# Optimization experiments

Measured on AMD Instinct MI355X. Metric: run time of the kernel, lower is better.

The kernel has to match this reference:

```python
import jax, jax.numpy as jnp
import numpy as np

DAYS = 10
EPS = 1e-5


def _ln(x, g, b, axis):
    # LayerNorm over a single axis with affine params of shape (x.shape[axis],)
    m = x.mean(axis=axis, keepdims=True)
    v = ((x - m) ** 2).mean(axis=axis, keepdims=True)
    xn = (x - m) * jax.lax.rsqrt(v + EPS)
    shp = [1] * x.ndim
    shp[axis] = x.shape[axis]
    return xn * g.reshape(shp) + b.reshape(shp)


def setup_inputs() -> dict:
    B, T, C = 8192, 30, 64
    H = 30  # lstm hidden
    P = C * (C - 1) // 2  # 2016 pairwise channels
    CH1 = 2 * P + 5 * C + 7 * C  # 4800
    ks = jax.random.split(jax.random.key(0), 16)
    s = 0.05
    x = jax.random.uniform(ks[0], (B, T, C), dtype=jnp.float32, minval=0.5, maxval=1.5)
    inp = {
        'x': x,
        'ln_ts_g': jnp.ones((7, 3), jnp.float32),
        'ln_ts_b': jnp.zeros((7, 3), jnp.float32),
        'pe_w': jax.random.normal(ks[1], (7 * C, C, DAYS), jnp.float32) * s,
        'pe_b': jnp.zeros((7 * C,), jnp.float32),
        'pe_g': jnp.ones((3,), jnp.float32),
        'pe_beta': jnp.zeros((3,), jnp.float32),
        'enc1_w': jax.random.normal(ks[2], (CH1 // 2, CH1), jnp.float32) * s,
        'enc1_b': jnp.zeros((CH1 // 2,), jnp.float32),
        'enc1_g': jnp.ones((3,), jnp.float32),
        'enc1_bb': jnp.zeros((3,), jnp.float32),
        'enc2_w': jax.random.normal(ks[3], (CH1 // 4, CH1 // 2), jnp.float32) * s,
        'enc2_b': jnp.zeros((CH1 // 4,), jnp.float32),
        'enc2_g': jnp.ones((3,), jnp.float32),
        'enc2_bb': jnp.zeros((3,), jnp.float32),
        'enc3_w': jax.random.normal(ks[4], (CH1 // 8, CH1 // 4), jnp.float32) * s,
        'enc3_b': jnp.zeros((CH1 // 8,), jnp.float32),
        'enc3_g': jnp.ones((3,), jnp.float32),
        'enc3_bb': jnp.zeros((3,), jnp.float32),
        'enc4_w': jax.random.normal(ks[5], (CH1 // 16, CH1 // 8), jnp.float32) * s,
        'enc4_b': jnp.zeros((CH1 // 16,), jnp.float32),
        'enc4_g': jnp.ones((3,), jnp.float32),
        'enc4_bb': jnp.zeros((3,), jnp.float32),
        'w_ih': jax.random.normal(ks[6], (4 * H, CH1 // 16), jnp.float32) * s,
        'w_hh': jax.random.normal(ks[7], (4 * H, H), jnp.float32) * s,
        'b_ih': jnp.zeros((4 * H,), jnp.float32),
        'b_hh': jnp.zeros((4 * H,), jnp.float32),
        'ln2_g': jnp.ones((3,), jnp.float32),
        'ln2_b': jnp.zeros((3,), jnp.float32),
        'lin_w': jax.random.normal(ks[8], (1, 3 * H), jnp.float32) * s,
        'lin_b': jnp.zeros((1,), jnp.float32),
    }
    return inp


def reference(x, ln_ts_g, ln_ts_b, pe_w, pe_b, pe_g, pe_beta,
              enc1_w, enc1_b, enc1_g, enc1_bb,
              enc2_w, enc2_b, enc2_g, enc2_bb,
              enc3_w, enc3_b, enc3_g, enc3_bb,
              enc4_w, enc4_b, enc4_g, enc4_bb,
              w_ih, w_hh, b_ih, b_hh, ln2_g, ln2_b, lin_w, lin_b):
    B, T, C = x.shape
    W = T // DAYS  # 3 windows
    xw = x.reshape(B, W, DAYS, C)  # non-overlapping windows (stride == days)
    mu = xw.mean(2)                                    # (B,W,C)  TS_Mean
    xc = xw - mu[:, :, None, :]
    std = jnp.sqrt((xc * xc).sum(2) / (DAYS - 1))      # (B,W,C)  TS_Stddev (unbiased)
    covf = jnp.einsum('bwdi,bwdj->bwij', xc, xc) / (DAYS - 1)
    iu, ju = np.triu_indices(C, 1)
    cov = covf[:, :, iu, ju]                           # (B,W,P)  TS_Cov
    corr = cov / (std[:, :, iu] * std[:, :, ju])       # (B,W,P)  TS_Corr
    zscore = mu / std                                  # TS_Zscore
    ret = xw[:, :, -1, :] / xw[:, :, 0, :] - 1.0       # TS_Return
    dw = jnp.arange(1, DAYS + 1, dtype=x.dtype)
    dw = dw / dw.sum()
    decay = jnp.einsum('bwdc,d->bwc', xw, dw)          # TS_Decaylinear
    branches = [corr, cov, std, zscore, ret, decay, mu]
    # per-branch TS_LayerNorm1d over the time axis (size W=3)
    feats = [_ln(br, ln_ts_g[k], ln_ts_b[k], axis=1) for k, br in enumerate(branches)]
    xfeat = jnp.concatenate(feats, axis=2).transpose(0, 2, 1)  # (B, 2P+5C, W)
    # param_extraction: Conv1d(C, 7C, k=10, s=10) + LayerNorm(W)
    pe = jnp.einsum('bwdc,ocd->bow', xw, pe_w) + pe_b[None, :, None]
    pe = _ln(pe, pe_g, pe_beta, axis=2)                # (B, 7C, W)
    h = jnp.concatenate([xfeat, pe], axis=1)           # (B, ch1, W)
    for w_, b_, g_, bb_ in ((enc1_w, enc1_b, enc1_g, enc1_bb),
                            (enc2_w, enc2_b, enc2_g, enc2_bb),
                            (enc3_w, enc3_b, enc3_g, enc3_bb),
                            (enc4_w, enc4_b, enc4_g, enc4_bb)):
        h = jax.nn.relu(_ln(jnp.einsum('oc,bcw->bow', w_, h) + b_[None, :, None], g_, bb_, axis=2))
    # LSTM over W=3 steps, batch_first
    seq = h.transpose(2, 0, 1)  # (W, B, ch2)
    Hn = w_hh.shape[1]

    def step(carry, xt):
        hp, cp = carry
        gates = xt @ w_ih.T + b_ih + hp @ w_hh.T + b_hh
        i, f, g, o = jnp.split(gates, 4, axis=-1)
        c = jax.nn.sigmoid(f) * cp + jax.nn.sigmoid(i) * jnp.tanh(g)
        hn = jax.nn.sigmoid(o) * jnp.tanh(c)
        return (hn, c), hn

    h0 = jnp.zeros((seq.shape[1], Hn), x.dtype)
    _, ys = jax.lax.scan(step, (h0, h0), seq)          # (W,B,Hn)
    lo = ys.transpose(1, 2, 0)                         # (B,Hn,W)
    lo = _ln(lo, ln2_g, ln2_b, axis=2).reshape(B, -1)  # (B, 3*Hn)
    return lo @ lin_w.T + lin_b                        # (B,1)
```

## Files before the change

kernel.cpp:

```cpp
#include <hip/hip_runtime.h>
#include <cstdint>
#include <cstddef>

#define EPS_LN 1e-5f

constexpr int TB = 30;
constexpr int CC = 64;
constexpr int DD = 10;
constexpr int WN = 3;
constexpr int PP = 2016;
constexpr int F1 = 4352;
constexpr int PEO = 448;
constexpr int CH = 4800;

typedef unsigned short u16;
typedef __attribute__((ext_vector_type(8))) short short8;
typedef __attribute__((ext_vector_type(4))) float f32x4;

__device__ __forceinline__ float sigm(float x) { return 1.f / (1.f + expf(-x)); }

__device__ __forceinline__ u16 f2bf(float v) {
    union { float f; uint32_t u; } c; c.f = v;
    uint32_t u = c.u;
    uint32_t r = (u + 0x7FFFu + ((u >> 16) & 1u)) >> 16;
    return (u16)r;
}
__device__ __forceinline__ float bf2f(u16 h) {
    union { uint32_t u; float f; } c; c.u = ((uint32_t)h) << 16;
    return c.f;
}
__device__ __forceinline__ void store_split(u16* __restrict__ hi, u16* __restrict__ lo,
                                            size_t idx, float v) {
    u16 h = f2bf(v);
    hi[idx] = h;
    lo[idx] = f2bf(v - bf2f(h));
}

__device__ __forceinline__ void gll16(const void* g, void* l) {
    __builtin_amdgcn_global_load_lds((const __attribute__((address_space(1))) void*)g,
                                     (__attribute__((address_space(3))) void*)l, 16, 0, 0);
}

__global__ __launch_bounds__(256)
void feat_kernel(const float* __restrict__ x,
                 const float* __restrict__ ln_ts_g, const float* __restrict__ ln_ts_b,
                 const float* __restrict__ pe_w, const float* __restrict__ pe_b,
                 const float* __restrict__ pe_g, const float* __restrict__ pe_beta,
                 u16* __restrict__ hh, u16* __restrict__ hl)
{
    __shared__ float xs[TB * CC];
    __shared__ float mu[WN * CC], sd[WN * CC];
    __shared__ float lg[21], lb[21], pg[3], pb2[3];

    const int tid = threadIdx.x;
    const int b = blockIdx.x;
    const float* xb = x + (size_t)b * (TB * CC);

    for (int i = tid; i < TB * CC; i += 256) xs[i] = xb[i];
    if (tid < 21) { lg[tid] = ln_ts_g[tid]; lb[tid] = ln_ts_b[tid]; }
    if (tid >= 32 && tid < 35) { pg[tid - 32] = pe_g[tid - 32]; pb2[tid - 32] = pe_beta[tid - 32]; }
    __syncthreads();

    if (tid < WN * CC) {
        int w = tid / CC, c = tid % CC;
        float s = 0.f;
#pragma unroll
        for (int d = 0; d < DD; ++d) s += xs[(w * DD + d) * CC + c];
        float m = s * (1.f / DD);
        float q = 0.f;
#pragma unroll
        for (int d = 0; d < DD; ++d) { float t = xs[(w * DD + d) * CC + c] - m; q += t * t; }
        mu[tid] = m;
        sd[tid] = sqrtf(q * (1.f / (DD - 1)));
    }
    __syncthreads();

    const size_t nbase = (size_t)b * WN;

    auto ln3store = [&](float v0, float v1, float v2, int k, int col) {
        float m = (v0 + v1 + v2) * (1.f / 3.f);
        float d0 = v0 - m, d1 = v1 - m, d2 = v2 - m;
        float rs = 1.f / sqrtf((d0 * d0 + d1 * d1 + d2 * d2) * (1.f / 3.f) + EPS_LN);
        store_split(hh, hl, (nbase + 0) * CH + col, d0 * rs * lg[k * 3 + 0] + lb[k * 3 + 0]);
        store_split(hh, hl, (nbase + 1) * CH + col, d1 * rs * lg[k * 3 + 1] + lb[k * 3 + 1]);
        store_split(hh, hl, (nbase + 2) * CH + col, d2 * rs * lg[k * 3 + 2] + lb[k * 3 + 2]);
    };

    for (int p = tid; p < PP; p += 256) {
        int i = (int)((2 * CC - 1 - sqrtf((float)((2 * CC - 1) * (2 * CC - 1) - 8 * p))) * 0.5f);
        if (i < 0) i = 0;
        if (i > CC - 2) i = CC - 2;
        while (((i + 1) * (2 * CC - i - 2)) / 2 <= p) ++i;
        while ((i * (2 * CC - i - 1)) / 2 > p) --i;
        int j = i + 1 + (p - (i * (2 * CC - i - 1)) / 2);
        float cv[3], cr[3];
#pragma unroll
        for (int w = 0; w < WN; ++w) {
            float mi = mu[w * CC + i], mj = mu[w * CC + j];
            float s = 0.f;
#pragma unroll
            for (int d = 0; d < DD; ++d)
                s += (xs[(w * DD + d) * CC + i] - mi) * (xs[(w * DD + d) * CC + j] - mj);
            s *= (1.f / (DD - 1));
            cv[w] = s;
            cr[w] = s / (sd[w * CC + i] * sd[w * CC + j]);
        }
        ln3store(cr[0], cr[1], cr[2], 0, p);
        ln3store(cv[0], cv[1], cv[2], 1, PP + p);
    }

    for (int f = tid; f < 5 * CC; f += 256) {
        int k = 2 + f / CC;
        int c = f % CC;
        float v[3];
#pragma unroll
        for (int w = 0; w < WN; ++w) {
            float val;
            if (k == 2) val = sd[w * CC + c];
            else if (k == 3) val = mu[w * CC + c] / sd[w * CC + c];
            else if (k == 4) val = xs[(w * DD + DD - 1) * CC + c] / xs[(w * DD) * CC + c] - 1.f;
            else if (k == 5) {
                float s = 0.f;
#pragma unroll
                for (int d = 0; d < DD; ++d) s += xs[(w * DD + d) * CC + c] * (float)(d + 1);
                val = s * (1.f / 55.f);
            } else val = mu[w * CC + c];
            v[w] = val;
        }
        ln3store(v[0], v[1], v[2], k, 2 * PP + f);
    }

    for (int o = tid; o < PEO; o += 256) {
        const float* wr = pe_w + (size_t)o * (CC * DD);
        float v0 = 0.f, v1 = 0.f, v2 = 0.f;
        for (int c = 0; c < CC; ++c) {
#pragma unroll
            for (int d = 0; d < DD; ++d) {
                float wv = wr[c * DD + d];
                v0 += xs[(0 * DD + d) * CC + c] * wv;
                v1 += xs[(1 * DD + d) * CC + c] * wv;
                v2 += xs[(2 * DD + d) * CC + c] * wv;
            }
        }
        float bo = pe_b[o];
        v0 += bo; v1 += bo; v2 += bo;
        float m = (v0 + v1 + v2) * (1.f / 3.f);
        float d0 = v0 - m, d1 = v1 - m, d2 = v2 - m;
        float rs = 1.f / sqrtf((d0 * d0 + d1 * d1 + d2 * d2) * (1.f / 3.f) + EPS_LN);
        store_split(hh, hl, (nbase + 0) * CH + F1 + o, d0 * rs * pg[0] + pb2[0]);
        store_split(hh, hl, (nbase + 1) * CH + F1 + o, d1 * rs * pg[1] + pb2[1]);
        store_split(hh, hl, (nbase + 2) * CH + F1 + o, d2 * rs * pg[2] + pb2[2]);
    }
}

__global__ __launch_bounds__(256)
void wconv_ker(const float* __restrict__ W, int O, int K, int Kpad,
               u16* __restrict__ Wh, u16* __restrict__ Wl)
{
    int idx = blockIdx.x * 256 + threadIdx.x;
    if (idx >= O * Kpad) return;
    int o = idx / Kpad, k = idx - o * Kpad;
    float v = (k < K) ? W[(size_t)o * K + k] : 0.f;
    u16 h = f2bf(v);
    Wh[idx] = h;
    Wl[idx] = f2bf(v - bf2f(h));
}

template<bool FUSE>
__global__ __launch_bounds__(256)
void gemm_mfma(const u16* __restrict__ Whi, const u16* __restrict__ Wlo,
               const u16* __restrict__ Xhi, const u16* __restrict__ Xlo,
               const float* __restrict__ bias,
               const float* __restrict__ lng, const float* __restrict__ lnb,
               int O, int Kpad, int N, int Ntrip, int Opad,
               u16* __restrict__ Oh, u16* __restrict__ Ol,
               float* __restrict__ Yf)
{
    union SMem {
        struct { u16 A[128 * 64]; u16 B[128 * 64]; } s;
        float L[128][68];
    };
    __shared__ SMem sm;

    const int tid = threadIdx.x;
    const int o0 = blockIdx.x * 128;
    const int n0 = blockIdx.y * 126;
    const int T0 = blockIdx.y * 42;

    const int w  = tid >> 6;
    const int wn = w >> 1, wo = w & 1;
    const int l  = tid & 63;
    const int lr = l & 15, lhi = l >> 4;
    const int rg = l >> 3, sl = l & 7;
    const int ck = sl ^ rg;

    f32x4 acc[4][4];
#pragma unroll
    for (int m = 0; m < 4; ++m)
#pragma unroll
        for (int n = 0; n < 4; ++n) acc[m][n] = (f32x4)0.f;

    for (int k0 = 0; k0 < Kpad; k0 += 32) {
#pragma unroll
        for (int j = 0; j < 8; ++j) {
            int blk = j * 4 + w;
            if (blk < 16) {
                int row = blk * 8 + rg;
                size_t gb = (size_t)(n0 + row) * Kpad + k0;
                const u16* src = (ck < 4) ? (Xhi + gb + ck * 8) : (Xlo + gb + (ck - 4) * 8);
                gll16(src, &sm.s.A[blk * 512]);
            } else {
                int row = (blk - 16) * 8 + rg;
                size_t gb = (size_t)(o0 + row) * Kpad + k0;
                const u16* src = (ck < 4) ? (Whi + gb + ck * 8) : (Wlo + gb + (ck - 4) * 8);
                gll16(src, &sm.s.B[(blk - 16) * 512]);
            }
        }
        __syncthreads();

        short8 ah[4], al[4], bh[4], bl[4];
#pragma unroll
        for (int m = 0; m < 4; ++m) {
            int r = wn * 64 + m * 16 + lr;
            int shi = lhi ^ (r & 7);
            int slo = (4 ^ lhi) ^ (r & 7);
            ah[m] = *reinterpret_cast<const short8*>(&sm.s.A[r * 64 + shi * 8]);
            al[m] = *reinterpret_cast<const short8*>(&sm.s.A[r * 64 + slo * 8]);
        }
#pragma unroll
        for (int n = 0; n < 4; ++n) {
            int r = wo * 64 + n * 16 + lr;
            int shi = lhi ^ (r & 7);
            int slo = (4 ^ lhi) ^ (r & 7);
            bh[n] = *reinterpret_cast<const short8*>(&sm.s.B[r * 64 + shi * 8]);
            bl[n] = *reinterpret_cast<const short8*>(&sm.s.B[r * 64 + slo * 8]);
        }
#pragma unroll
        for (int m = 0; m < 4; ++m)
#pragma unroll
            for (int n = 0; n < 4; ++n) {
                acc[m][n] = __builtin_amdgcn_mfma_f32_16x16x32_bf16(ah[m], bh[n], acc[m][n], 0, 0, 0);
                acc[m][n] = __builtin_amdgcn_mfma_f32_16x16x32_bf16(ah[m], bl[n], acc[m][n], 0, 0, 0);
                acc[m][n] = __builtin_amdgcn_mfma_f32_16x16x32_bf16(al[m], bh[n], acc[m][n], 0, 0, 0);
            }
        __syncthreads();
    }

    float bv[4];
#pragma unroll
    for (int nf = 0; nf < 4; ++nf) {
        int o = o0 + wo * 64 + nf * 16 + lr;
        bv[nf] = (o < O) ? bias[o] : 0.f;
    }

    if constexpr (!FUSE) {
#pragma unroll
        for (int nf = 0; nf < 4; ++nf) {
            int o = o0 + wo * 64 + nf * 16 + lr;
            if (o >= O) continue;
#pragma unroll
            for (int m = 0; m < 4; ++m) {
                int nb = n0 + wn * 64 + m * 16 + lhi * 4;
#pragma unroll
                for (int r = 0; r < 4; ++r) {
                    int n = nb + r;
                    if (n < N) Yf[(size_t)n * O + o] = acc[m][nf][r] + bv[nf];
                }
            }
        }
    } else {
        const float g0 = lng[0], g1 = lng[1], g2 = lng[2];
        const float q0 = lnb[0], q1 = lnb[1], q2 = lnb[2];
        for (int h = 0; h < 2; ++h) {
            __syncthreads();
            if (wo == h) {
#pragma unroll
                for (int m = 0; m < 4; ++m)
#pragma unroll
                    for (int nf = 0; nf < 4; ++nf)
#pragma unroll
                        for (int r = 0; r < 4; ++r)
                            sm.L[wn * 64 + m * 16 + lhi * 4 + r][nf * 16 + lr] = acc[m][nf][r] + bv[nf];
            }
            __syncthreads();
            for (int it = 0; it < 11; ++it) {
                int item = it * 256 + tid;
                if (item < 42 * 64) {
                    int tl = item >> 6, c2 = item & 63;
                    int t = T0 + tl;
                    int o = o0 + h * 64 + c2;
                    if (t < Ntrip && o < Opad) {
                        size_t base = (size_t)(3 * t) * Opad + o;
                        if (o >= O) {
                            Oh[base] = 0; Ol[base] = 0;
                            Oh[base + Opad] = 0; Ol[base + Opad] = 0;
                            Oh[base + 2 * (size_t)Opad] = 0; Ol[base + 2 * (size_t)Opad] = 0;
                        } else {
                            float y0 = sm.L[3 * tl + 0][c2];
                            float y1 = sm.L[3 * tl + 1][c2];
                            float y2 = sm.L[3 * tl + 2][c2];
                            float mm = (y0 + y1 + y2) * (1.f / 3.f);
                            float d0 = y0 - mm, d1 = y1 - mm, d2 = y2 - mm;
                            float rs = 1.f / sqrtf((d0 * d0 + d1 * d1 + d2 * d2) * (1.f / 3.f) + EPS_LN);
                            store_split(Oh, Ol, base,                    fmaxf(d0 * rs * g0 + q0, 0.f));
                            store_split(Oh, Ol, base + Opad,             fmaxf(d1 * rs * g1 + q1, 0.f));
                            store_split(Oh, Ol, base + 2 * (size_t)Opad, fmaxf(d2 * rs * g2 + q2, 0.f));
                        }
                    }
                }
            }
        }
    }
}

__global__ __launch_bounds__(256)
void lstm_ker(const float* __restrict__ gates,
              const float* __restrict__ w_hh, const float* __restrict__ b_hh,
              const float* __restrict__ ln2g, const float* __restrict__ ln2b,
              const float* __restrict__ lin_w, const float* __restrict__ lin_b,
              float* __restrict__ out, int Bc)
{
    __shared__ float whh[120 * 30];
    __shared__ float bhh[120];
    __shared__ float lw[90];
    __shared__ float lg[3], lbv[3];
    __shared__ float hbuf[8][32];

    const int tid = threadIdx.x;
    for (int i = tid; i < 3600; i += 256) whh[i] = w_hh[i];
    if (tid < 120) bhh[tid] = b_hh[tid];
    if (tid < 90) lw[tid] = lin_w[tid];
    if (tid < 3) { lg[tid] = ln2g[tid]; lbv[tid] = ln2b[tid]; }

    const int g = tid >> 5;
    const int u = tid & 31;
    const int bl = blockIdx.x * 8 + g;

    hbuf[g][u] = 0.f;
    __syncthreads();

    float cstate = 0.f;
    float y0 = 0.f, y1 = 0.f, y2 = 0.f;

#pragma unroll
    for (int t = 0; t < 3; ++t) {
        float hn = 0.f;
        if (u < 30) {
            const float* gr = gates + (size_t)(bl * 3 + t) * 120;
            float gi = gr[u]      + bhh[u];
            float gf = gr[30 + u] + bhh[30 + u];
            float gg = gr[60 + u] + bhh[60 + u];
            float go = gr[90 + u] + bhh[90 + u];
            for (int v = 0; v < 30; ++v) {
                float hv = hbuf[g][v];
                gi += whh[u * 30 + v] * hv;
                gf += whh[(30 + u) * 30 + v] * hv;
                gg += whh[(60 + u) * 30 + v] * hv;
                go += whh[(90 + u) * 30 + v] * hv;
            }
            float cn = sigm(gf) * cstate + sigm(gi) * tanhf(gg);
            cstate = cn;
            hn = sigm(go) * tanhf(cn);
        }
        __syncthreads();
        if (u < 30) hbuf[g][u] = hn;
        __syncthreads();
        if (t == 0) y0 = hn; else if (t == 1) y1 = hn; else y2 = hn;
    }

    float acc = 0.f;
    if (u < 30) {
        float m = (y0 + y1 + y2) * (1.f / 3.f);
        float d0 = y0 - m, d1 = y1 - m, d2 = y2 - m;
        float rs = 1.f / sqrtf((d0 * d0 + d1 * d1 + d2 * d2) * (1.f / 3.f) + EPS_LN);
        acc  = (d0 * rs * lg[0] + lbv[0]) * lw[u * 3 + 0];
        acc += (d1 * rs * lg[1] + lbv[1]) * lw[u * 3 + 1];
        acc += (d2 * rs * lg[2] + lbv[2]) * lw[u * 3 + 2];
    }
#pragma unroll
    for (int off = 16; off > 0; off >>= 1)
        acc += __shfl_down(acc, off, 32);
    if (u == 0) out[bl] = acc + lin_b[0];
}

extern "C" void kernel_launch(void* const* d_in, const int* in_sizes, int n_in,
                              void* d_out, int out_size, void* d_ws, size_t ws_size,
                              hipStream_t stream)
{
    const float* x       = (const float*)d_in[0];
    const float* ln_ts_g = (const float*)d_in[1];
    const float* ln_ts_b = (const float*)d_in[2];
    const float* pe_w    = (const float*)d_in[3];
    const float* pe_b    = (const float*)d_in[4];
    const float* pe_g    = (const float*)d_in[5];
    const float* pe_beta = (const float*)d_in[6];
    const float* e1w = (const float*)d_in[7];  const float* e1b  = (const float*)d_in[8];
    const float* e1g = (const float*)d_in[9];  const float* e1bb = (const float*)d_in[10];
    const float* e2w = (const float*)d_in[11]; const float* e2b  = (const float*)d_in[12];
    const float* e2g = (const float*)d_in[13]; const float* e2bb = (const float*)d_in[14];
    const float* e3w = (const float*)d_in[15]; const float* e3b  = (const float*)d_in[16];
    const float* e3g = (const float*)d_in[17]; const float* e3bb = (const float*)d_in[18];
    const float* e4w = (const float*)d_in[19]; const float* e4b  = (const float*)d_in[20];
    const float* e4g = (const float*)d_in[21]; const float* e4bb = (const float*)d_in[22];
    const float* w_ih = (const float*)d_in[23];
    const float* w_hh = (const float*)d_in[24];
    const float* b_ih = (const float*)d_in[25];
    const float* b_hh = (const float*)d_in[26];
    const float* ln2g = (const float*)d_in[27];
    const float* ln2b = (const float*)d_in[28];
    const float* lin_w = (const float*)d_in[29];
    const float* lin_b = (const float*)d_in[30];
    float* out = (float*)d_out;

    const int Btot = 8192;

    const int LO[5]  = {2400, 1200, 600, 300, 120};
    const int LK[5]  = {4800, 2400, 1200, 600, 300};
    const int LKP[5] = {4800, 2400, 1216, 608, 320};
    const float* LW[5] = {e1w, e2w, e3w, e4w, w_ih};

    u16* wp = (u16*)d_ws;
    u16* Wh[5]; u16* Wl[5];
    size_t wcount = 0;
    for (int i = 0; i < 5; ++i) {
        Wh[i] = wp + wcount; wcount += (size_t)LO[i] * LKP[i];
        Wl[i] = wp + wcount; wcount += (size_t)LO[i] * LKP[i];
    }
    const size_t wbytes = wcount * sizeof(u16);

    const size_t per_b = (size_t)3 * 4800 * 2 * 2 + (size_t)3 * 2400 * 2 * 2 + (size_t)3 * 128 * 4;
    const size_t slack = (size_t)128 * (4800 + 2400) * 2 * 2 + 4096;
    int Bc = 2048;
    while (Bc > 128 && wbytes + slack + (size_t)Bc * per_b > ws_size) Bc >>= 1;
    const int n_chunks = Btot / Bc;
    const int N = Bc * 3;

    u16* Xah = wp + wcount;            wcount += (size_t)(N + 128) * 4800;
    u16* Xal = wp + wcount;            wcount += (size_t)(N + 128) * 4800;
    u16* Xbh = wp + wcount;            wcount += (size_t)(N + 128) * 2400;
    u16* Xbl = wp + wcount;            wcount += (size_t)(N + 128) * 2400;
    float* Yf = (float*)(wp + wcount);

    for (int i = 0; i < 5; ++i) {
        int tot = LO[i] * LKP[i];
        wconv_ker<<<(tot + 255) / 256, 256, 0, stream>>>(LW[i], LO[i], LK[i], LKP[i], Wh[i], Wl[i]);
    }

    const int GY = (N + 125) / 126;

    for (int c = 0; c < n_chunks; ++c) {
        const int b0 = c * Bc;
        feat_kernel<<<Bc, 256, 0, stream>>>(x + (size_t)b0 * TB * CC,
                                            ln_ts_g, ln_ts_b, pe_w, pe_b, pe_g, pe_beta,
                                            Xah, Xal);

        gemm_mfma<true><<<dim3(19, GY), 256, 0, stream>>>(
            Wh[0], Wl[0], Xah, Xal, e1b, e1g, e1bb,
            2400, 4800, N, Bc, 2400, Xbh, Xbl, nullptr);

        gemm_mfma<true><<<dim3(10, GY), 256, 0, stream>>>(
            Wh[1], Wl[1], Xbh, Xbl, e2b, e2g, e2bb,
            1200, 2400, N, Bc, 1216, Xah, Xal, nullptr);

        gemm_mfma<true><<<dim3(5, GY), 256, 0, stream>>>(
            Wh[2], Wl[2], Xah, Xal, e3b, e3g, e3bb,
            600, 1216, N, Bc, 608, Xbh, Xbl, nullptr);

        gemm_mfma<true><<<dim3(3, GY), 256, 0, stream>>>(
            Wh[3], Wl[3], Xbh, Xbl, e4b, e4g, e4bb,
            300, 608, N, Bc, 320, Xah, Xal, nullptr);

        gemm_mfma<false><<<dim3(1, GY), 256, 0, stream>>>(
            Wh[4], Wl[4], Xah, Xal, b_ih, nullptr, nullptr,
            120, 320, N, Bc, 120, nullptr, nullptr, Yf);

        lstm_ker<<<Bc / 8, 256, 0, stream>>>(Yf, w_hh, b_hh, ln2g, ln2b,
                                             lin_w, lin_b, out + b0, Bc);
    }
}
```

Baseline: 5.759 ms.

## Remap GEMM blocks across XCDs and split hi/lo shared-memory tiles

Switches the GEMM launch to a 1D grid and remaps block IDs so consecutive tiles are grouped onto the same XCD, aiming for better L2 reuse of weight and activation tiles on the multi-die MI355X. It also replaces the XOR-swizzled combined hi/lo shared layout with four separate unswizzled 32-column buffers, which simplifies addressing. The unswizzled 64-byte row stride may bring back LDS bank conflicts on the fragment reads.

```diff
diff --git a/kernel.cpp b/kernel.cpp
--- a/kernel.cpp
+++ b/kernel.cpp
@@ -172,27 +172,35 @@
                const u16* __restrict__ Xhi, const u16* __restrict__ Xlo,
                const float* __restrict__ bias,
                const float* __restrict__ lng, const float* __restrict__ lnb,
-               int O, int Kpad, int N, int Ntrip, int Opad,
+               int O, int Kpad, int N, int Ntrip, int Opad, int GX,
                u16* __restrict__ Oh, u16* __restrict__ Ol,
                float* __restrict__ Yf)
 {
     union SMem {
-        struct { u16 A[128 * 64]; u16 B[128 * 64]; } s;
+        struct { u16 A0[128 * 32], A1[128 * 32], B0[128 * 32], B1[128 * 32]; } s;
         float L[128][68];
     };
     __shared__ SMem sm;
 
+    const int nwg = gridDim.x;
+    const int orig = blockIdx.x;
+    const int q = nwg >> 3, rb = nwg & 7;
+    const int xcd = orig & 7, idx = orig >> 3;
+    const int wg = (xcd < rb ? xcd * (q + 1) : rb * (q + 1) + (xcd - rb) * q) + idx;
+    const int bx = wg % GX;
+    const int by = wg / GX;
+
     const int tid = threadIdx.x;
-    const int o0 = blockIdx.x * 128;
-    const int n0 = blockIdx.y * 126;
-    const int T0 = blockIdx.y * 42;
+    const int o0 = bx * 128;
+    const int n0 = by * 126;
+    const int T0 = by * 42;
 
     const int w  = tid >> 6;
     const int wn = w >> 1, wo = w & 1;
     const int l  = tid & 63;
     const int lr = l & 15, lhi = l >> 4;
-    const int rg = l >> 3, sl = l & 7;
-    const int ck = sl ^ rg;
+    const int srow = l >> 2;
+    const int sc8  = (l & 3) * 8;
 
     f32x4 acc[4][4];
 #pragma unroll
@@ -204,16 +212,20 @@
 #pragma unroll
         for (int j = 0; j < 8; ++j) {
             int blk = j * 4 + w;
-            if (blk < 16) {
-                int row = blk * 8 + rg;
-                size_t gb = (size_t)(n0 + row) * Kpad + k0;
-                const u16* src = (ck < 4) ? (Xhi + gb + ck * 8) : (Xlo + gb + (ck - 4) * 8);
-                gll16(src, &sm.s.A[blk * 512]);
+            int grp = blk & 7;
+            int row = grp * 16 + srow;
+            if (blk < 8) {
+                size_t g = (size_t)(n0 + row) * Kpad + k0 + sc8;
+                gll16(Xhi + g, &sm.s.A0[grp * 512]);
+            } else if (blk < 16) {
+                size_t g = (size_t)(n0 + row) * Kpad + k0 + sc8;
+                gll16(Xlo + g, &sm.s.A1[grp * 512]);
+            } else if (blk < 24) {
+                size_t g = (size_t)(o0 + row) * Kpad + k0 + sc8;
+                gll16(Whi + g, &sm.s.B0[grp * 512]);
             } else {
-                int row = (blk - 16) * 8 + rg;
-                size_t gb = (size_t)(o0 + row) * Kpad + k0;
-                const u16* src = (ck < 4) ? (Whi + gb + ck * 8) : (Wlo + gb + (ck - 4) * 8);
-                gll16(src, &sm.s.B[(blk - 16) * 512]);
+                size_t g = (size_t)(o0 + row) * Kpad + k0 + sc8;
+                gll16(Wlo + g, &sm.s.B1[grp * 512]);
             }
         }
         __syncthreads();
@@ -222,18 +234,14 @@
 #pragma unroll
         for (int m = 0; m < 4; ++m) {
             int r = wn * 64 + m * 16 + lr;
-            int shi = lhi ^ (r & 7);
-            int slo = (4 ^ lhi) ^ (r & 7);
-            ah[m] = *reinterpret_cast<const short8*>(&sm.s.A[r * 64 + shi * 8]);
-            al[m] = *reinterpret_cast<const short8*>(&sm.s.A[r * 64 + slo * 8]);
+            ah[m] = *reinterpret_cast<const short8*>(&sm.s.A0[r * 32 + lhi * 8]);
+            al[m] = *reinterpret_cast<const short8*>(&sm.s.A1[r * 32 + lhi * 8]);
         }
 #pragma unroll
         for (int n = 0; n < 4; ++n) {
             int r = wo * 64 + n * 16 + lr;
-            int shi = lhi ^ (r & 7);
-            int slo = (4 ^ lhi) ^ (r & 7);
-            bh[n] = *reinterpret_cast<const short8*>(&sm.s.B[r * 64 + shi * 8]);
-            bl[n] = *reinterpret_cast<const short8*>(&sm.s.B[r * 64 + slo * 8]);
+            bh[n] = *reinterpret_cast<const short8*>(&sm.s.B0[r * 32 + lhi * 8]);
+            bl[n] = *reinterpret_cast<const short8*>(&sm.s.B1[r * 32 + lhi * 8]);
         }
 #pragma unroll
         for (int m = 0; m < 4; ++m)
@@ -454,25 +462,25 @@
                                             ln_ts_g, ln_ts_b, pe_w, pe_b, pe_g, pe_beta,
                                             Xah, Xal);
 
-        gemm_mfma<true><<<dim3(19, GY), 256, 0, stream>>>(
+        gemm_mfma<true><<<19 * GY, 256, 0, stream>>>(
             Wh[0], Wl[0], Xah, Xal, e1b, e1g, e1bb,
-            2400, 4800, N, Bc, 2400, Xbh, Xbl, nullptr);
-
-        gemm_mfma<true><<<dim3(10, GY), 256, 0, stream>>>(
+            2400, 4800, N, Bc, 2400, 19, Xbh, Xbl, nullptr);
+
+        gemm_mfma<true><<<10 * GY, 256, 0, stream>>>(
             Wh[1], Wl[1], Xbh, Xbl, e2b, e2g, e2bb,
-            1200, 2400, N, Bc, 1216, Xah, Xal, nullptr);
-
-        gemm_mfma<true><<<dim3(5, GY), 256, 0, stream>>>(
+            1200, 2400, N, Bc, 1216, 10, Xah, Xal, nullptr);
+
+        gemm_mfma<true><<<5 * GY, 256, 0, stream>>>(
             Wh[2], Wl[2], Xah, Xal, e3b, e3g, e3bb,
-            600, 1216, N, Bc, 608, Xbh, Xbl, nullptr);
-
-        gemm_mfma<true><<<dim3(3, GY), 256, 0, stream>>>(
+            600, 1216, N, Bc, 608, 5, Xbh, Xbl, nullptr);
+
+        gemm_mfma<true><<<3 * GY, 256, 0, stream>>>(
             Wh[3], Wl[3], Xbh, Xbl, e4b, e4g, e4bb,
-            300, 608, N, Bc, 320, Xah, Xal, nullptr);
-
-        gemm_mfma<false><<<dim3(1, GY), 256, 0, stream>>>(
+            300, 608, N, Bc, 320, 3, Xah, Xal, nullptr);
+
+        gemm_mfma<false><<<1 * GY, 256, 0, stream>>>(
             Wh[4], Wl[4], Xah, Xal, b_ih, nullptr, nullptr,
-            120, 320, N, Bc, 120, nullptr, nullptr, Yf);
+            120, 320, N, Bc, 120, 1, nullptr, nullptr, Yf);
 
         lstm_ker<<<Bc / 8, 256, 0, stream>>>(Yf, w_hh, b_hh, ln2g, ln2b,
                                              lin_w, lin_b, out + b0, Bc);
```

Result: slower. 8.427 ms (+46.3%).
